# Kernel optimization log

Measured on AMD Instinct MI355X. Metric: run time of the kernel, lower is better.

Reference implementation:

```python
import jax, jax.numpy as jnp
import numpy as np

EPS = 1e-8
SCALE = 23.0
LEAKY_SLOPE = 0.01  # torch nn.LeakyReLU default

M, B, D = 65536, 2048, 13
H1, H2, H3 = 300, 600, 100


def _linear_params(key, out_f, in_f):
    # torch nn.Linear default init: U(-1/sqrt(in), 1/sqrt(in))
    k1, k2 = jax.random.split(key)
    bound = 1.0 / np.sqrt(in_f)
    W = jax.random.uniform(k1, (out_f, in_f), jnp.float32, -bound, bound)
    b = jax.random.uniform(k2, (out_f,), jnp.float32, -bound, bound)
    return W, b


def setup_inputs() -> dict:
    key = jax.random.key(0)
    ks = jax.random.split(key, 6)
    memory = jax.random.normal(ks[0], (M, D), jnp.float32)
    value = jax.random.normal(ks[1], (B, D), jnp.float32)
    W1, b1 = _linear_params(ks[2], H1, D)
    W2, b2 = _linear_params(ks[3], H2, H1)
    W3, b3 = _linear_params(ks[4], H3, H2)
    W4, b4 = _linear_params(ks[5], D, H3)
    return {"memory": memory, "value": value,
            "W1": W1, "b1": b1, "W2": W2, "b2": b2,
            "W3": W3, "b3": b3, "W4": W4, "b4": b4}


def _mlp(x, W1, b1, W2, b2, W3, b3, W4, b4):
    h = jax.nn.relu(x @ W1.T + b1)                      # [M, 300]
    h = jax.nn.leaky_relu(h @ W2.T + b2, LEAKY_SLOPE)   # [M, 600]
    h = jax.nn.relu(h @ W3.T + b3)                      # [M, 100]
    return jax.nn.leaky_relu(h @ W4.T + b4, LEAKY_SLOPE)  # [M, 13]


def reference(memory, value, W1, b1, W2, b2, W3, b3, W4, b4):
    # abstract_memory = self.net(self.memory)
    t1 = _mlp(memory, W1, b1, W2, b2, W3, b3, W4, b4)   # [M, 13]
    t2 = value.reshape(value.shape[0], -1)              # flatten(value, 1) -> [B, 13]
    # cosine similarity with torch eps clamping on each norm
    t1n = t1 / jnp.maximum(jnp.linalg.norm(t1, axis=-1, keepdims=True), EPS)
    t2n = t2 / jnp.maximum(jnp.linalg.norm(t2, axis=-1, keepdims=True), EPS)
    s = (t2n @ t1n.T) * SCALE                           # [B, M], replaces per-row python loop
    return jnp.max(s, axis=1)                           # [B]
```

## Files before the change

kernel.cpp:

```cpp
#include <hip/hip_runtime.h>


typedef __bf16 bf16x8 __attribute__((ext_vector_type(8)));
typedef float f32x16 __attribute__((ext_vector_type(16)));

constexpr size_t OFF_W1B = 0;
constexpr size_t OFF_W2B = 10240;
constexpr size_t OFF_W3B = 419840;
constexpr size_t OFF_W4B = 583680;
constexpr size_t OFF_T2N = 591872;
constexpr size_t OFF_T1N = 657408;
constexpr size_t OFF_PART= 2754560;

__device__ __forceinline__ bf16x8 ld8(const __bf16* p) {
    return *reinterpret_cast<const bf16x8*>(p);
}
__device__ __forceinline__ f32x16 mfma32(bf16x8 a, bf16x8 b, f32x16 c) {
    return __builtin_amdgcn_mfma_f32_32x32x16_bf16(a, b, c, 0, 0, 0);
}

__device__ __forceinline__ void cvtswap(const f32x16& a, bf16x8& f0, bf16x8& f1) {
    unsigned w[8];
    #pragma unroll
    for (int j = 0; j < 8; j++)
        asm("v_cvt_pk_bf16_f32 %0, %1, %2" : "=v"(w[j]) : "v"(a[2*j]), "v"(a[2*j+1]));
    unsigned a0 = w[0], b0 = w[2]; asm("v_permlane32_swap_b32 %0, %1" : "+v"(a0), "+v"(b0));
    unsigned a1 = w[1], b1 = w[3]; asm("v_permlane32_swap_b32 %0, %1" : "+v"(a1), "+v"(b1));
    unsigned a2 = w[4], b2 = w[6]; asm("v_permlane32_swap_b32 %0, %1" : "+v"(a2), "+v"(b2));
    unsigned a3 = w[5], b3 = w[7]; asm("v_permlane32_swap_b32 %0, %1" : "+v"(a3), "+v"(b3));
    union { unsigned u[4]; bf16x8 v; } p, q;
    p.u[0] = a0; p.u[1] = a1; p.u[2] = b0; p.u[3] = b1; f0 = p.v;
    q.u[0] = a2; q.u[1] = a3; q.u[2] = b2; q.u[3] = b3; f1 = q.v;
}

__global__ void prep_kernel(const float* __restrict__ W1, const float* __restrict__ b1,
                            const float* __restrict__ W2, const float* __restrict__ b2,
                            const float* __restrict__ W3, const float* __restrict__ b3,
                            const float* __restrict__ W4, const float* __restrict__ b4,
                            const float* __restrict__ value, char* __restrict__ ws) {
    __bf16* W1B = (__bf16*)(ws + OFF_W1B);
    __bf16* W2B = (__bf16*)(ws + OFF_W2B);
    __bf16* W3B = (__bf16*)(ws + OFF_W3B);
    __bf16* W4B = (__bf16*)(ws + OFF_W4B);
    __bf16* T2N = (__bf16*)(ws + OFF_T2N);

    int idx = blockIdx.x * 256 + threadIdx.x;
    if (idx < 5120) {
        int e = idx & 7, lane = (idx >> 3) & 63, nt = idx >> 9;
        int n = nt*32 + (lane & 31);
        int k = (lane >> 5)*8 + e;
        float v = 0.0f;
        if (n < 300)       v = (k < 13) ? W1[n*13 + k] : (k == 13 ? b1[n] : 0.0f);
        else if (n == 300) v = (k == 13) ? 1.0f : 0.0f;
        W1B[idx] = (__bf16)v;
        return;
    }
    idx -= 5120;
    if (idx < 204800) {
        int e = idx & 7, lane = (idx >> 3) & 63, r = idx >> 9;
        int ks = r % 20, nt = r / 20;
        int n = nt*32 + (lane & 31);
        int k = ks*16 + (lane >> 5)*8 + e;
        float v = 0.0f;
        if (n < 600)       v = (k < 300) ? W2[n*300 + k] : (k == 300 ? b2[n] : 0.0f);
        else if (n == 600) v = (k == 300) ? 1.0f : 0.0f;
        W2B[idx] = (__bf16)v;
        return;
    }
    idx -= 204800;
    if (idx < 81920) {
        int e = idx & 7, lane = (idx >> 3) & 63, r = idx >> 9;
        int ks = r % 40, nt = r / 40;
        int n = nt*32 + (lane & 31);
        int k = ks*16 + (lane >> 5)*8 + e;
        float v = 0.0f;
        if (n < 100)       v = (k < 600) ? W3[n*600 + k] : (k == 600 ? b3[n] : 0.0f);
        else if (n == 100) v = (k == 600) ? 1.0f : 0.0f;
        W3B[idx] = (__bf16)v;
        return;
    }
    idx -= 81920;
    if (idx < 4096) {
        int e = idx & 7, lane = (idx >> 3) & 63, ks = idx >> 9;
        int n = lane & 31;
        int k = ks*16 + (lane >> 5)*8 + e;
        float v = 0.0f;
        if (n < 13) v = (k < 100) ? W4[n*100 + k] : (k == 100 ? b4[n] : 0.0f);
        W4B[idx] = (__bf16)v;
        return;
    }
    idx -= 4096;
    if (idx < 2048) {
        float v[13]; float s = 0.0f;
        #pragma unroll
        for (int k = 0; k < 13; k++) { v[k] = value[idx*13 + k]; s += v[k]*v[k]; }
        float inv = 1.0f / fmaxf(sqrtf(s), 1e-8f);
        #pragma unroll
        for (int k = 0; k < 13; k++) T2N[idx*16 + k] = (__bf16)(v[k] * inv);
        #pragma unroll
        for (int k = 13; k < 16; k++) T2N[idx*16 + k] = (__bf16)0.0f;
    }
}

__global__ __launch_bounds__(256, 2) void mlp_kernel(const float* __restrict__ mem,
                                                     char* __restrict__ ws) {
    __shared__ float t1s[128*13];

    const __bf16* W1B = (const __bf16*)(ws + OFF_W1B);
    const __bf16* W2B = (const __bf16*)(ws + OFF_W2B);
    const __bf16* W3B = (const __bf16*)(ws + OFF_W3B);
    const __bf16* W4B = (const __bf16*)(ws + OFF_W4B);
    __bf16* T1N = (__bf16*)(ws + OFF_T1N);

    const int tid = threadIdx.x;
    const int wave = tid >> 6, lane = tid & 63;
    const int l31 = lane & 31, hi = lane >> 5;
    const int bm0 = blockIdx.x * 128;
    const int m = bm0 + wave*32 + l31;

    bf16x8 xf;
    {
        union { __bf16 h[8]; bf16x8 v; } u;
        const float* xr = mem + (size_t)m*13;
        if (hi == 0) {
            #pragma unroll
            for (int e = 0; e < 8; e++) u.h[e] = (__bf16)xr[e];
        } else {
            #pragma unroll
            for (int e = 0; e < 5; e++) u.h[e] = (__bf16)xr[8 + e];
            u.h[5] = (__bf16)1.0f;
            u.h[6] = (__bf16)0.0f;
            u.h[7] = (__bf16)0.0f;
        }
        xf = u.v;
    }

    bf16x8 afc[20];
    #pragma unroll
    for (int nt = 0; nt < 10; nt++) {
        bf16x8 wf = ld8(W1B + (size_t)nt*512 + lane*8);
        f32x16 z = {};
        f32x16 a = mfma32(wf, xf, z);
        #pragma unroll
        for (int r = 0; r < 16; r++) a[r] = fmaxf(a[r], 0.0f);
        cvtswap(a, afc[2*nt], afc[2*nt + 1]);
    }

    f32x16 acc3[4] = {};
    for (int nt2 = 0; nt2 < 20; nt2++) {
        bf16x8 wf3[8];
        #pragma unroll
        for (int n3 = 0; n3 < 4; n3++) {
            const __bf16* bp3 = W3B + ((size_t)(n3*40 + 2*nt2)*64 + lane)*8;
            wf3[2*n3]     = ld8(bp3);
            wf3[2*n3 + 1] = ld8(bp3 + 512);
        }
        const __bf16* bp2 = W2B + (size_t)nt2*10240 + lane*8;
        f32x16 e0 = {}, e1 = {};
        #pragma unroll
        for (int ks = 0; ks < 20; ks += 2) {
            e0 = mfma32(ld8(bp2 + ks*512),       afc[ks],     e0);
            e1 = mfma32(ld8(bp2 + (ks + 1)*512), afc[ks + 1], e1);
        }
        #pragma unroll
        for (int r = 0; r < 16; r++) {
            float v = e0[r] + e1[r];
            e0[r] = fmaxf(v, 0.0f) + 0.01f*fminf(v, 0.0f);
        }
        bf16x8 h2f0, h2f1;
        cvtswap(e0, h2f0, h2f1);
        #pragma unroll
        for (int n3 = 0; n3 < 4; n3++) {
            acc3[n3] = mfma32(wf3[2*n3],     h2f0, acc3[n3]);
            acc3[n3] = mfma32(wf3[2*n3 + 1], h2f1, acc3[n3]);
        }
    }

    f32x16 acc4 = {};
    #pragma unroll
    for (int n3 = 0; n3 < 4; n3++) {
        f32x16 h;
        #pragma unroll
        for (int r = 0; r < 16; r++) h[r] = fmaxf(acc3[n3][r], 0.0f);
        bf16x8 f0, f1;
        cvtswap(h, f0, f1);
        acc4 = mfma32(ld8(W4B + (size_t)(2*n3)*512 + lane*8),     f0, acc4);
        acc4 = mfma32(ld8(W4B + (size_t)(2*n3 + 1)*512 + lane*8), f1, acc4);
    }
    const int mrow = wave*32 + l31;
    #pragma unroll
    for (int r = 0; r < 16; r++) {
        const int n4 = (r & 3) + 8*(r >> 2) + 4*hi;
        if (n4 < 13) {
            float v = acc4[r];
            t1s[mrow*13 + n4] = fmaxf(v, 0.0f) + 0.01f*fminf(v, 0.0f);
        }
    }
    __syncthreads();

    if (tid < 128) {
        float s = 0.0f, v[13];
        #pragma unroll
        for (int k = 0; k < 13; k++) { v[k] = t1s[tid*13 + k]; s += v[k]*v[k]; }
        const float inv = 1.0f / fmaxf(sqrtf(s), 1e-8f);
        union { __bf16 o[16]; bf16x8 f[2]; } u;
        #pragma unroll
        for (int k = 0; k < 13; k++) u.o[k] = (__bf16)(v[k] * inv);
        #pragma unroll
        for (int k = 13; k < 16; k++) u.o[k] = (__bf16)0.0f;
        bf16x8* dst = reinterpret_cast<bf16x8*>(T1N + (size_t)(bm0 + tid)*16);
        dst[0] = u.f[0];
        dst[1] = u.f[1];
    }
}

__global__ __launch_bounds__(256) void sim_kernel(const char* __restrict__ ws_c,
                                                  float* __restrict__ part) {
    const char* ws = ws_c;
    const __bf16* T1N = (const __bf16*)(ws + OFF_T1N);
    const __bf16* T2N = (const __bf16*)(ws + OFF_T2N);
    const int wave = threadIdx.x >> 6, lane = threadIdx.x & 63;
    const int l31 = lane & 31, hi = lane >> 5;
    const int bgroup = blockIdx.x & 15, ms = blockIdx.x >> 4;
    const int b0 = (bgroup*4 + wave) * 32;

    const bf16x8 af = ld8(T2N + (size_t)(b0 + l31)*16 + hi*8);
    const f32x16 zero = {};
    f32x16 mx;
    #pragma unroll
    for (int r = 0; r < 16; r++) mx[r] = -3.0e38f;

    #pragma unroll 4
    for (int mt = ms; mt < 2048; mt += 128) {
        bf16x8 bf0 = ld8(T1N + ((size_t)mt*32 + l31)*16 + hi*8);
        bf16x8 bf1 = ld8(T1N + ((size_t)(mt + 64)*32 + l31)*16 + hi*8);
        f32x16 d0 = mfma32(af, bf0, zero);
        f32x16 d1 = mfma32(af, bf1, zero);
        #pragma unroll
        for (int r = 0; r < 16; r++)
            mx[r] = fmaxf(mx[r], fmaxf(d0[r], d1[r]));
    }
    #pragma unroll
    for (int off = 1; off <= 16; off <<= 1) {
        #pragma unroll
        for (int r = 0; r < 16; r++) mx[r] = fmaxf(mx[r], __shfl_xor(mx[r], off));
    }
    if (l31 == 0) {
        #pragma unroll
        for (int reg = 0; reg < 16; reg++)
            part[ms*2048 + b0 + (reg & 3) + 8*(reg >> 2) + 4*hi] = mx[reg];
    }
}

__global__ void reduce_kernel(const float* __restrict__ part, float* __restrict__ out) {
    int b = blockIdx.x*256 + threadIdx.x;
    if (b < 2048) {
        float m = part[b];
        #pragma unroll
        for (int ms = 1; ms < 64; ms++) m = fmaxf(m, part[ms*2048 + b]);
        out[b] = 23.0f * m;
    }
}

extern "C" void kernel_launch(void* const* d_in, const int* in_sizes, int n_in,
                              void* d_out, int out_size, void* d_ws, size_t ws_size,
                              hipStream_t stream) {
    const float* memory = (const float*)d_in[0];
    const float* value  = (const float*)d_in[1];
    const float* W1 = (const float*)d_in[2]; const float* b1 = (const float*)d_in[3];
    const float* W2 = (const float*)d_in[4]; const float* b2 = (const float*)d_in[5];
    const float* W3 = (const float*)d_in[6]; const float* b3 = (const float*)d_in[7];
    const float* W4 = (const float*)d_in[8]; const float* b4 = (const float*)d_in[9];
    char* ws = (char*)d_ws;
    float* part = (float*)(ws + OFF_PART);
    float* out = (float*)d_out;

    prep_kernel<<<1164, 256, 0, stream>>>(W1, b1, W2, b2, W3, b3, W4, b4, value, ws);
    mlp_kernel<<<512, 256, 0, stream>>>(memory, ws);
    sim_kernel<<<1024, 256, 0, stream>>>(ws, part);
    reduce_kernel<<<8, 256, 0, stream>>>(part, out);
}
```

Before: 137.2 us.

## Process two 32-row tiles per wave in MLP kernel to reuse weight loads

Each wave now handles 64 memory rows, two MFMA row tiles, instead of 32. Every W1/W2/W3/W4 fragment loaded from global memory now feeds two MFMAs, which halves weight traffic per row and gives more independent MFMA chains. The grid drops to 256 blocks with launch bounds of 1 block per CU, and a per-iteration s_barrier is added to keep waves in step for cache reuse. The cost is roughly doubled register pressure (two 20-fragment activation sets and doubled accumulators), lower occupancy, and only 256 blocks, which may underfill the CUs.

```diff
diff --git a/kernel.cpp b/kernel.cpp
--- a/kernel.cpp
+++ b/kernel.cpp
@@ -102,9 +102,9 @@
     }
 }
 
-__global__ __launch_bounds__(256, 2) void mlp_kernel(const float* __restrict__ mem,
+__global__ __launch_bounds__(256, 1) void mlp_kernel(const float* __restrict__ mem,
                                                      char* __restrict__ ws) {
-    __shared__ float t1s[128*13];
+    __shared__ float t1s[256*13];
 
     const __bf16* W1B = (const __bf16*)(ws + OFF_W1B);
     const __bf16* W2B = (const __bf16*)(ws + OFF_W2B);
@@ -115,38 +115,48 @@
     const int tid = threadIdx.x;
     const int wave = tid >> 6, lane = tid & 63;
     const int l31 = lane & 31, hi = lane >> 5;
-    const int bm0 = blockIdx.x * 128;
-    const int m = bm0 + wave*32 + l31;
-
-    bf16x8 xf;
+    const int bm0 = blockIdx.x * 256;
+    const int mA = bm0 + wave*64 + l31;
+    const int mB = mA + 32;
+
+    bf16x8 xfA, xfB;
     {
         union { __bf16 h[8]; bf16x8 v; } u;
-        const float* xr = mem + (size_t)m*13;
+        const float* xr = mem + (size_t)mA*13;
+        const float* yr = mem + (size_t)mB*13;
         if (hi == 0) {
             #pragma unroll
             for (int e = 0; e < 8; e++) u.h[e] = (__bf16)xr[e];
+            xfA = u.v;
+            #pragma unroll
+            for (int e = 0; e < 8; e++) u.h[e] = (__bf16)yr[e];
+            xfB = u.v;
         } else {
             #pragma unroll
             for (int e = 0; e < 5; e++) u.h[e] = (__bf16)xr[8 + e];
-            u.h[5] = (__bf16)1.0f;
-            u.h[6] = (__bf16)0.0f;
-            u.h[7] = (__bf16)0.0f;
-        }
-        xf = u.v;
-    }
-
-    bf16x8 afc[20];
+            u.h[5] = (__bf16)1.0f; u.h[6] = (__bf16)0.0f; u.h[7] = (__bf16)0.0f;
+            xfA = u.v;
+            #pragma unroll
+            for (int e = 0; e < 5; e++) u.h[e] = (__bf16)yr[8 + e];
+            u.h[5] = (__bf16)1.0f; u.h[6] = (__bf16)0.0f; u.h[7] = (__bf16)0.0f;
+            xfB = u.v;
+        }
+    }
+
+    bf16x8 afcA[20], afcB[20];
     #pragma unroll
     for (int nt = 0; nt < 10; nt++) {
         bf16x8 wf = ld8(W1B + (size_t)nt*512 + lane*8);
         f32x16 z = {};
-        f32x16 a = mfma32(wf, xf, z);
-        #pragma unroll
-        for (int r = 0; r < 16; r++) a[r] = fmaxf(a[r], 0.0f);
-        cvtswap(a, afc[2*nt], afc[2*nt + 1]);
-    }
-
-    f32x16 acc3[4] = {};
+        f32x16 aA = mfma32(wf, xfA, z);
+        f32x16 aB = mfma32(wf, xfB, z);
+        #pragma unroll
+        for (int r = 0; r < 16; r++) { aA[r] = fmaxf(aA[r], 0.0f); aB[r] = fmaxf(aB[r], 0.0f); }
+        cvtswap(aA, afcA[2*nt], afcA[2*nt + 1]);
+        cvtswap(aB, afcB[2*nt], afcB[2*nt + 1]);
+    }
+
+    f32x16 acc3A[4] = {}, acc3B[4] = {};
     for (int nt2 = 0; nt2 < 20; nt2++) {
         bf16x8 wf3[8];
         #pragma unroll
@@ -156,49 +166,69 @@
             wf3[2*n3 + 1] = ld8(bp3 + 512);
         }
         const __bf16* bp2 = W2B + (size_t)nt2*10240 + lane*8;
-        f32x16 e0 = {}, e1 = {};
+        f32x16 eA0 = {}, eA1 = {}, eB0 = {}, eB1 = {};
         #pragma unroll
         for (int ks = 0; ks < 20; ks += 2) {
-            e0 = mfma32(ld8(bp2 + ks*512),       afc[ks],     e0);
-            e1 = mfma32(ld8(bp2 + (ks + 1)*512), afc[ks + 1], e1);
+            bf16x8 w0 = ld8(bp2 + ks*512);
+            bf16x8 w1 = ld8(bp2 + (ks + 1)*512);
+            eA0 = mfma32(w0, afcA[ks],     eA0);
+            eB0 = mfma32(w0, afcB[ks],     eB0);
+            eA1 = mfma32(w1, afcA[ks + 1], eA1);
+            eB1 = mfma32(w1, afcB[ks + 1], eB1);
         }
         #pragma unroll
         for (int r = 0; r < 16; r++) {
-            float v = e0[r] + e1[r];
-            e0[r] = fmaxf(v, 0.0f) + 0.01f*fminf(v, 0.0f);
-        }
-        bf16x8 h2f0, h2f1;
-        cvtswap(e0, h2f0, h2f1);
+            float vA = eA0[r] + eA1[r];
+            float vB = eB0[r] + eB1[r];
+            eA0[r] = fmaxf(vA, 0.0f) + 0.01f*fminf(vA, 0.0f);
+            eB0[r] = fmaxf(vB, 0.0f) + 0.01f*fminf(vB, 0.0f);
+        }
+        bf16x8 hA0, hA1, hB0, hB1;
+        cvtswap(eA0, hA0, hA1);
+        cvtswap(eB0, hB0, hB1);
         #pragma unroll
         for (int n3 = 0; n3 < 4; n3++) {
-            acc3[n3] = mfma32(wf3[2*n3],     h2f0, acc3[n3]);
-            acc3[n3] = mfma32(wf3[2*n3 + 1], h2f1, acc3[n3]);
-        }
-    }
-
-    f32x16 acc4 = {};
+            acc3A[n3] = mfma32(wf3[2*n3],     hA0, acc3A[n3]);
+            acc3A[n3] = mfma32(wf3[2*n3 + 1], hA1, acc3A[n3]);
+            acc3B[n3] = mfma32(wf3[2*n3],     hB0, acc3B[n3]);
+            acc3B[n3] = mfma32(wf3[2*n3 + 1], hB1, acc3B[n3]);
+        }
+        __builtin_amdgcn_s_barrier();
+    }
+
+    f32x16 acc4A = {}, acc4B = {};
     #pragma unroll
     for (int n3 = 0; n3 < 4; n3++) {
-        f32x16 h;
-        #pragma unroll
-        for (int r = 0; r < 16; r++) h[r] = fmaxf(acc3[n3][r], 0.0f);
-        bf16x8 f0, f1;
-        cvtswap(h, f0, f1);
-        acc4 = mfma32(ld8(W4B + (size_t)(2*n3)*512 + lane*8),     f0, acc4);
-        acc4 = mfma32(ld8(W4B + (size_t)(2*n3 + 1)*512 + lane*8), f1, acc4);
-    }
-    const int mrow = wave*32 + l31;
+        f32x16 hA, hB;
+        #pragma unroll
+        for (int r = 0; r < 16; r++) {
+            hA[r] = fmaxf(acc3A[n3][r], 0.0f);
+            hB[r] = fmaxf(acc3B[n3][r], 0.0f);
+        }
+        bf16x8 fA0, fA1, fB0, fB1;
+        cvtswap(hA, fA0, fA1);
+        cvtswap(hB, fB0, fB1);
+        bf16x8 w0 = ld8(W4B + (size_t)(2*n3)*512 + lane*8);
+        bf16x8 w1 = ld8(W4B + (size_t)(2*n3 + 1)*512 + lane*8);
+        acc4A = mfma32(w0, fA0, acc4A);
+        acc4A = mfma32(w1, fA1, acc4A);
+        acc4B = mfma32(w0, fB0, acc4B);
+        acc4B = mfma32(w1, fB1, acc4B);
+    }
+    const int rA = wave*64 + l31, rB = rA + 32;
     #pragma unroll
     for (int r = 0; r < 16; r++) {
         const int n4 = (r & 3) + 8*(r >> 2) + 4*hi;
         if (n4 < 13) {
-            float v = acc4[r];
-            t1s[mrow*13 + n4] = fmaxf(v, 0.0f) + 0.01f*fminf(v, 0.0f);
+            float vA = acc4A[r];
+            float vB = acc4B[r];
+            t1s[rA*13 + n4] = fmaxf(vA, 0.0f) + 0.01f*fminf(vA, 0.0f);
+            t1s[rB*13 + n4] = fmaxf(vB, 0.0f) + 0.01f*fminf(vB, 0.0f);
         }
     }
     __syncthreads();
 
-    if (tid < 128) {
+    {
         float s = 0.0f, v[13];
         #pragma unroll
         for (int k = 0; k < 13; k++) { v[k] = t1s[tid*13 + k]; s += v[k]*v[k]; }
@@ -276,7 +306,7 @@
     float* out = (float*)d_out;
 
     prep_kernel<<<1164, 256, 0, stream>>>(W1, b1, W2, b2, W3, b3, W4, b4, value, ws);
-    mlp_kernel<<<512, 256, 0, stream>>>(memory, ws);
+    mlp_kernel<<<256, 256, 0, stream>>>(memory, ws);
     sim_kernel<<<1024, 256, 0, stream>>>(ws, part);
     reduce_kernel<<<8, 256, 0, stream>>>(part, out);
 }
```

New measurement: 176.0 us. 1.28x slower.
